# Kernel optimization log

Hardware: AMD Instinct MI355X
Metric: run time of the kernel (lower is better)

## Reference

```python
import jax, jax.numpy as jnp
import numpy as np

N_TOKEN = 1024
FFN_MULT = 4
B = 32
D = 1024
LN_EPS = 1e-5


def _layer_norm(x, gamma, beta):
    mu = jnp.mean(x, axis=-1, keepdims=True)
    var = jnp.var(x, axis=-1, keepdims=True)
    return (x - mu) * jax.lax.rsqrt(var + LN_EPS) * gamma + beta


def setup_inputs() -> dict:
    key = jax.random.key(0)
    ks = jax.random.split(key, 12)
    n, m = N_TOKEN, FFN_MULT * N_TOKEN
    s_in = 1.0 / np.sqrt(n)
    s_ff = 1.0 / np.sqrt(m)
    return {
        "Q": jax.random.normal(ks[0], (B, n), jnp.float32),
        "K": jax.random.normal(ks[1], (B, n, D), jnp.float32),
        "V": jax.random.normal(ks[2], (B, n, D), jnp.float32),
        "mu_w": jax.random.uniform(ks[3], (n, n), jnp.float32, -s_in, s_in),
        "mu_b": jax.random.uniform(ks[4], (n,), jnp.float32, -s_in, s_in),
        "sigma_w": jax.random.uniform(ks[5], (n, n), jnp.float32, -s_in, s_in),
        "sigma_b": jax.random.uniform(ks[6], (n,), jnp.float32, -s_in, s_in),
        "ffn_w1": jax.random.uniform(ks[7], (m, n), jnp.float32, -s_in, s_in),
        "ffn_b1": jax.random.uniform(ks[8], (m,), jnp.float32, -s_in, s_in),
        "ffn_w2": jax.random.uniform(ks[9], (n, m), jnp.float32, -s_ff, s_ff),
        "ffn_b2": jax.random.uniform(ks[10], (n,), jnp.float32, -s_ff, s_ff),
        "ln_ff_g": jnp.ones((n,), jnp.float32),
        "ln_ff_b": jnp.zeros((n,), jnp.float32),
        "ln_q_g": jnp.ones((n,), jnp.float32),
        "ln_q_b": jnp.zeros((n,), jnp.float32),
    }


def reference(Q, K, V, mu_w, mu_b, sigma_w, sigma_b, ffn_w1, ffn_b1,
              ffn_w2, ffn_b2, ln_ff_g, ln_ff_b, ln_q_g, ln_q_b):
    q = _layer_norm(Q, ln_q_g, ln_q_b)                       # (B, n)
    mu = jnp.tanh(q @ mu_w.T + mu_b)[..., None]              # (B, n, 1)
    sigma = (q @ sigma_w.T + sigma_b)[..., None]             # (B, n, 1)
    # Gaussian-kernel pseudo-attention: broadcast over D then reduce
    S = jnp.exp(-0.5 * (K - mu) ** 2 / (sigma ** 2 + 1e-8))  # (B, n, D)
    A = jnp.sum(S * V, axis=-1)                              # (B, n)
    x = A + Q
    h = _layer_norm(x, ln_ff_g, ln_ff_b)
    h = jax.nn.silu(h @ ffn_w1.T + ffn_b1) @ ffn_w2.T + ffn_b2
    return x + h
```

## Files before the change

### kernel.cpp

```cpp
#include <hip/hip_runtime.h>

#define N_TOK  1024
#define D_DIM  1024
#define M_FFN  4096

__device__ __forceinline__ float wave_reduce(float v) {
    #pragma unroll
    for (int off = 32; off > 0; off >>= 1) v += __shfl_xor(v, off);
    return v;
}

__global__ void ln_kernel(const float* __restrict__ X,
                          const float* __restrict__ gam,
                          const float* __restrict__ bet,
                          float* __restrict__ Y) {
    int b = blockIdx.x, t = threadIdx.x;
    float4 x = ((const float4*)(X + (size_t)b * N_TOK))[t];
    float s = x.x + x.y + x.z + x.w;
    float q = x.x*x.x + x.y*x.y + x.z*x.z + x.w*x.w;
    s = wave_reduce(s); q = wave_reduce(q);
    __shared__ float sa[4], sb[4];
    int wid = t >> 6;
    if ((t & 63) == 0) { sa[wid] = s; sb[wid] = q; }
    __syncthreads();
    float ts = sa[0] + sa[1] + sa[2] + sa[3];
    float tq = sb[0] + sb[1] + sb[2] + sb[3];
    float mean = ts * (1.f / N_TOK);
    float var  = tq * (1.f / N_TOK) - mean * mean;
    float rs = rsqrtf(var + 1e-5f);
    float4 g4 = ((const float4*)gam)[t];
    float4 b4 = ((const float4*)bet)[t];
    float4 o;
    o.x = (x.x - mean) * rs * g4.x + b4.x;
    o.y = (x.y - mean) * rs * g4.y + b4.y;
    o.z = (x.z - mean) * rs * g4.z + b4.z;
    o.w = (x.w - mean) * rs * g4.w + b4.w;
    ((float4*)(Y + (size_t)b * N_TOK))[t] = o;
}

__global__ void gemm_tn_kernel(const float* __restrict__ A,
                               const float* __restrict__ W0,
                               const float* __restrict__ W1,
                               float* __restrict__ C0,
                               float* __restrict__ C1,
                               int N, int K, int kchunk) {
    int t = threadIdx.x;
    int lane = t & 63;
    int wv = t >> 6;
    int n = blockIdx.x * 64 + lane;
    int k0 = blockIdx.y * kchunk;
    const float* W = blockIdx.z ? W1 : W0;
    float*      Cc = blockIdx.z ? C1 : C0;
    const float* wp = W + (size_t)n * K + k0;
    const float* ap = A + k0;
    float acc[8] = {0.f,0.f,0.f,0.f,0.f,0.f,0.f,0.f};
    for (int k = 0; k < kchunk; k += 4) {
        float4 w4 = *(const float4*)(wp + k);
        #pragma unroll
        for (int j = 0; j < 8; j++) {
            int m = wv * 8 + j;
            float4 a4 = *(const float4*)(ap + (size_t)m * K + k);
            acc[j] += w4.x*a4.x + w4.y*a4.y + w4.z*a4.z + w4.w*a4.w;
        }
    }
    #pragma unroll
    for (int j = 0; j < 8; j++)
        atomicAdd(Cc + (size_t)(wv * 8 + j) * N + n, acc[j]);
}

__global__ void attn_kernel(const float* __restrict__ Kp,
                            const float* __restrict__ Vp,
                            const float* __restrict__ Qp,
                            const float* __restrict__ mu_acc,
                            const float* __restrict__ sg_acc,
                            const float* __restrict__ mu_b,
                            const float* __restrict__ sg_b,
                            float* __restrict__ xo) {
    int t = threadIdx.x;
    int row = blockIdx.x * 4 + (t >> 6);
    int lane = t & 63;
    int i = row & (N_TOK - 1);
    const float4* kr = (const float4*)(Kp + (size_t)row * D_DIM);
    const float4* vr = (const float4*)(Vp + (size_t)row * D_DIM);
    float4 k4[4], v4[4];
    #pragma unroll
    for (int c = 0; c < 4; c++) k4[c] = kr[c * 64 + lane];
    #pragma unroll
    for (int c = 0; c < 4; c++) v4[c] = vr[c * 64 + lane];
    float mu = tanhf(mu_acc[row] + mu_b[i]);
    float sg = sg_acc[row] + sg_b[i];
    float coef = -0.5f / (sg * sg + 1e-8f);
    float acc = 0.f;
    #pragma unroll
    for (int c = 0; c < 4; c++) {
        float d;
        d = k4[c].x - mu; acc += __expf(coef * d * d) * v4[c].x;
        d = k4[c].y - mu; acc += __expf(coef * d * d) * v4[c].y;
        d = k4[c].z - mu; acc += __expf(coef * d * d) * v4[c].z;
        d = k4[c].w - mu; acc += __expf(coef * d * d) * v4[c].w;
    }
    acc = wave_reduce(acc);
    if (lane == 0) xo[row] = acc + Qp[row];
}

__global__ void silu_kernel(const float* __restrict__ acc,
                            const float* __restrict__ b1,
                            float* __restrict__ g) {
    int idx = blockIdx.x * 256 + threadIdx.x;
    float z = acc[idx] + b1[idx & (M_FFN - 1)];
    g[idx] = z / (1.f + __expf(-z));
}

__global__ void final_kernel(const float* __restrict__ x,
                             const float* __restrict__ acc2,
                             const float* __restrict__ b2,
                             float* __restrict__ out) {
    int idx = blockIdx.x * 256 + threadIdx.x;
    out[idx] = x[idx] + acc2[idx] + b2[idx & (N_TOK - 1)];
}

extern "C" void kernel_launch(void* const* d_in, const int* in_sizes, int n_in,
                              void* d_out, int out_size, void* d_ws, size_t ws_size,
                              hipStream_t stream) {
    const float* Q       = (const float*)d_in[0];
    const float* Kp      = (const float*)d_in[1];
    const float* Vp      = (const float*)d_in[2];
    const float* mu_w    = (const float*)d_in[3];
    const float* mu_b    = (const float*)d_in[4];
    const float* sigma_w = (const float*)d_in[5];
    const float* sigma_b = (const float*)d_in[6];
    const float* w1      = (const float*)d_in[7];
    const float* b1      = (const float*)d_in[8];
    const float* w2      = (const float*)d_in[9];
    const float* b2      = (const float*)d_in[10];
    const float* ln_ff_g = (const float*)d_in[11];
    const float* ln_ff_b = (const float*)d_in[12];
    const float* ln_q_g  = (const float*)d_in[13];
    const float* ln_q_b  = (const float*)d_in[14];

    float* mu_acc = (float*)d_ws;
    float* sg_acc = mu_acc + 32768;
    float* f1_acc = sg_acc + 32768;
    float* f2_acc = f1_acc + 131072;
    float* xbuf   = f2_acc + 32768;
    float* qln    = xbuf   + 32768;
    float* h0     = qln    + 32768;
    float* g      = h0     + 32768;

    hipMemsetAsync(mu_acc, 0, (size_t)229376 * sizeof(float), stream);

    ln_kernel<<<32, 256, 0, stream>>>(Q, ln_q_g, ln_q_b, qln);

    gemm_tn_kernel<<<dim3(16, 16, 2), 256, 0, stream>>>(
        qln, mu_w, sigma_w, mu_acc, sg_acc, 1024, 1024, 64);

    attn_kernel<<<8192, 256, 0, stream>>>(Kp, Vp, Q, mu_acc, sg_acc,
                                          mu_b, sigma_b, xbuf);

    ln_kernel<<<32, 256, 0, stream>>>(xbuf, ln_ff_g, ln_ff_b, h0);

    gemm_tn_kernel<<<dim3(64, 8, 1), 256, 0, stream>>>(
        h0, w1, w1, f1_acc, f1_acc, 4096, 1024, 128);
    silu_kernel<<<512, 256, 0, stream>>>(f1_acc, b1, g);

    gemm_tn_kernel<<<dim3(16, 16, 1), 256, 0, stream>>>(
        g, w2, w2, f2_acc, f2_acc, 1024, 4096, 256);
    final_kernel<<<128, 256, 0, stream>>>(xbuf, f2_acc, b2, (float*)d_out);
}
```

Baseline: 400.2 us.

## Coalesce GEMM weight reads, fuse SiLU epilogue, and prefetch rows in attention

The GEMM kernel is restructured so that 16 lanes cooperate along K. Weight rows are now read as contiguous float4 segments, and a shuffle reduction replaces most split-K atomics. The first two GEMMs write results directly, with bias and SiLU fused into the FFN1 epilogue, which removes the separate silu kernel and most of the workspace memset. The attention kernel now handles four rows per wave and prefetches the next row's K/V into registers, which trades more register pressure for better latency hiding. With no split-K, the first two GEMMs launch fewer blocks and may run at lower occupancy.

```diff
diff --git a/kernel.cpp b/kernel.cpp
--- a/kernel.cpp
+++ b/kernel.cpp
@@ -38,34 +38,59 @@
     ((float4*)(Y + (size_t)b * N_TOK))[t] = o;
 }
 
-__global__ void gemm_tn_kernel(const float* __restrict__ A,
-                               const float* __restrict__ W0,
-                               const float* __restrict__ W1,
-                               float* __restrict__ C0,
-                               float* __restrict__ C1,
-                               int N, int K, int kchunk) {
+__global__ void gemm_kernel(const float* __restrict__ A,
+                            const float* __restrict__ W0,
+                            const float* __restrict__ W1,
+                            float* __restrict__ C0,
+                            float* __restrict__ C1,
+                            const float* __restrict__ bias,
+                            int N, int K, int kchunk, int mode) {
     int t = threadIdx.x;
-    int lane = t & 63;
-    int wv = t >> 6;
-    int n = blockIdx.x * 64 + lane;
-    int k0 = blockIdx.y * kchunk;
+    int lane = t & 63, wid = t >> 6;
+    int ksub = lane & 15, nsub = lane >> 4;
+    int mhalf = wid & 1, ngrp = wid >> 1;
+    int n = blockIdx.x * 8 + ngrp * 4 + nsub;
+    int k0 = blockIdx.y * kchunk + ksub * 4;
     const float* W = blockIdx.z ? W1 : W0;
-    float*      Cc = blockIdx.z ? C1 : C0;
+    float*       C = blockIdx.z ? C1 : C0;
     const float* wp = W + (size_t)n * K + k0;
-    const float* ap = A + k0;
-    float acc[8] = {0.f,0.f,0.f,0.f,0.f,0.f,0.f,0.f};
-    for (int k = 0; k < kchunk; k += 4) {
-        float4 w4 = *(const float4*)(wp + k);
+    const float* ap = A + (size_t)mhalf * 16 * K + k0;
+    float acc[16];
+    #pragma unroll
+    for (int j = 0; j < 16; j++) acc[j] = 0.f;
+    for (int kk = 0; kk < kchunk; kk += 64) {
+        float4 w4 = *(const float4*)(wp + kk);
         #pragma unroll
-        for (int j = 0; j < 8; j++) {
-            int m = wv * 8 + j;
-            float4 a4 = *(const float4*)(ap + (size_t)m * K + k);
-            acc[j] += w4.x*a4.x + w4.y*a4.y + w4.z*a4.z + w4.w*a4.w;
+        for (int j = 0; j < 16; j++) {
+            float4 a4 = *(const float4*)(ap + (size_t)j * K + kk);
+            acc[j] += a4.x*w4.x + a4.y*w4.y + a4.z*w4.z + a4.w*w4.w;
         }
     }
     #pragma unroll
-    for (int j = 0; j < 8; j++)
-        atomicAdd(Cc + (size_t)(wv * 8 + j) * N + n, acc[j]);
+    for (int j = 0; j < 16; j++) {
+        #pragma unroll
+        for (int off = 1; off < 16; off <<= 1)
+            acc[j] += __shfl_xor(acc[j], off);
+    }
+    if (ksub == 0) {
+        int mbase = mhalf * 16;
+        if (mode == 2) {
+            #pragma unroll
+            for (int j = 0; j < 16; j++)
+                atomicAdd(C + (size_t)(mbase + j) * N + n, acc[j]);
+        } else if (mode == 1) {
+            float bn = bias[n];
+            #pragma unroll
+            for (int j = 0; j < 16; j++) {
+                float z = acc[j] + bn;
+                C[(size_t)(mbase + j) * N + n] = z / (1.f + __expf(-z));
+            }
+        } else {
+            #pragma unroll
+            for (int j = 0; j < 16; j++)
+                C[(size_t)(mbase + j) * N + n] = acc[j];
+        }
+    }
 }
 
 __global__ void attn_kernel(const float* __restrict__ Kp,
@@ -77,38 +102,44 @@
                             const float* __restrict__ sg_b,
                             float* __restrict__ xo) {
     int t = threadIdx.x;
-    int row = blockIdx.x * 4 + (t >> 6);
-    int lane = t & 63;
-    int i = row & (N_TOK - 1);
-    const float4* kr = (const float4*)(Kp + (size_t)row * D_DIM);
-    const float4* vr = (const float4*)(Vp + (size_t)row * D_DIM);
-    float4 k4[4], v4[4];
+    int lane = t & 63, wid = t >> 6;
+    int row0 = blockIdx.x * 16 + wid * 4;
+    float4 ck[4], cv[4], nk[4], nv[4];
+    {
+        const float4* kp = (const float4*)(Kp + (size_t)row0 * D_DIM);
+        const float4* vp = (const float4*)(Vp + (size_t)row0 * D_DIM);
+        #pragma unroll
+        for (int c = 0; c < 4; c++) { ck[c] = kp[c * 64 + lane]; cv[c] = vp[c * 64 + lane]; }
+    }
     #pragma unroll
-    for (int c = 0; c < 4; c++) k4[c] = kr[c * 64 + lane];
-    #pragma unroll
-    for (int c = 0; c < 4; c++) v4[c] = vr[c * 64 + lane];
-    float mu = tanhf(mu_acc[row] + mu_b[i]);
-    float sg = sg_acc[row] + sg_b[i];
-    float coef = -0.5f / (sg * sg + 1e-8f);
-    float acc = 0.f;
-    #pragma unroll
-    for (int c = 0; c < 4; c++) {
-        float d;
-        d = k4[c].x - mu; acc += __expf(coef * d * d) * v4[c].x;
-        d = k4[c].y - mu; acc += __expf(coef * d * d) * v4[c].y;
-        d = k4[c].z - mu; acc += __expf(coef * d * d) * v4[c].z;
-        d = k4[c].w - mu; acc += __expf(coef * d * d) * v4[c].w;
+    for (int r = 0; r < 4; r++) {
+        int row = row0 + r;
+        if (r < 3) {
+            const float4* kp = (const float4*)(Kp + (size_t)(row + 1) * D_DIM);
+            const float4* vp = (const float4*)(Vp + (size_t)(row + 1) * D_DIM);
+            #pragma unroll
+            for (int c = 0; c < 4; c++) { nk[c] = kp[c * 64 + lane]; nv[c] = vp[c * 64 + lane]; }
+        }
+        int i = row & (N_TOK - 1);
+        float mu = tanhf(mu_acc[row] + mu_b[i]);
+        float sg = sg_acc[row] + sg_b[i];
+        float coef = -0.5f / (sg * sg + 1e-8f);
+        float acc = 0.f;
+        #pragma unroll
+        for (int c = 0; c < 4; c++) {
+            float d;
+            d = ck[c].x - mu; acc += __expf(coef * d * d) * cv[c].x;
+            d = ck[c].y - mu; acc += __expf(coef * d * d) * cv[c].y;
+            d = ck[c].z - mu; acc += __expf(coef * d * d) * cv[c].z;
+            d = ck[c].w - mu; acc += __expf(coef * d * d) * cv[c].w;
+        }
+        acc = wave_reduce(acc);
+        if (lane == 0) xo[row] = acc + Qp[row];
+        if (r < 3) {
+            #pragma unroll
+            for (int c = 0; c < 4; c++) { ck[c] = nk[c]; cv[c] = nv[c]; }
+        }
     }
-    acc = wave_reduce(acc);
-    if (lane == 0) xo[row] = acc + Qp[row];
-}
-
-__global__ void silu_kernel(const float* __restrict__ acc,
-                            const float* __restrict__ b1,
-                            float* __restrict__ g) {
-    int idx = blockIdx.x * 256 + threadIdx.x;
-    float z = acc[idx] + b1[idx & (M_FFN - 1)];
-    g[idx] = z / (1.f + __expf(-z));
 }
 
 __global__ void final_kernel(const float* __restrict__ x,
@@ -140,30 +171,28 @@
 
     float* mu_acc = (float*)d_ws;
     float* sg_acc = mu_acc + 32768;
-    float* f1_acc = sg_acc + 32768;
-    float* f2_acc = f1_acc + 131072;
+    float* f2_acc = sg_acc + 32768;
     float* xbuf   = f2_acc + 32768;
     float* qln    = xbuf   + 32768;
     float* h0     = qln    + 32768;
     float* g      = h0     + 32768;
 
-    hipMemsetAsync(mu_acc, 0, (size_t)229376 * sizeof(float), stream);
+    hipMemsetAsync(f2_acc, 0, (size_t)32768 * sizeof(float), stream);
 
     ln_kernel<<<32, 256, 0, stream>>>(Q, ln_q_g, ln_q_b, qln);
 
-    gemm_tn_kernel<<<dim3(16, 16, 2), 256, 0, stream>>>(
-        qln, mu_w, sigma_w, mu_acc, sg_acc, 1024, 1024, 64);
+    gemm_kernel<<<dim3(128, 1, 2), 256, 0, stream>>>(
+        qln, mu_w, sigma_w, mu_acc, sg_acc, nullptr, 1024, 1024, 1024, 0);
 
-    attn_kernel<<<8192, 256, 0, stream>>>(Kp, Vp, Q, mu_acc, sg_acc,
+    attn_kernel<<<2048, 256, 0, stream>>>(Kp, Vp, Q, mu_acc, sg_acc,
                                           mu_b, sigma_b, xbuf);
 
     ln_kernel<<<32, 256, 0, stream>>>(xbuf, ln_ff_g, ln_ff_b, h0);
 
-    gemm_tn_kernel<<<dim3(64, 8, 1), 256, 0, stream>>>(
-        h0, w1, w1, f1_acc, f1_acc, 4096, 1024, 128);
-    silu_kernel<<<512, 256, 0, stream>>>(f1_acc, b1, g);
+    gemm_kernel<<<dim3(512, 1, 1), 256, 0, stream>>>(
+        h0, w1, w1, g, g, b1, 4096, 1024, 1024, 1);
 
-    gemm_tn_kernel<<<dim3(16, 16, 1), 256, 0, stream>>>(
-        g, w2, w2, f2_acc, f2_acc, 1024, 4096, 256);
+    gemm_kernel<<<dim3(128, 2, 1), 256, 0, stream>>>(
+        g, w2, w2, f2_acc, f2_acc, nullptr, 1024, 4096, 2048, 2);
     final_kernel<<<128, 256, 0, stream>>>(xbuf, f2_acc, b2, (float*)d_out);
 }
```

Measured after the change: 420.1 us. 5.0% more time.
